# Kernel optimization log

Hardware: AMD Instinct MI355X
Metric: run time of the kernel (lower is better)

## Reference

```python
import jax, jax.numpy as jnp
import numpy as np

B, C, H, W, N = 4, 128, 240, 320, 1024
LEVEL = 8.0          # scaling[0] = 4 * img_scale with img_scale=2
E1_LAMDA = 1.0
E2_LAMDA = 2.0 / 7.0
GN_LAMDA = 0.3
EPS = 1e-9


def extract_features(f, coords):
    # f: (B,C,H,W); coords: (B,N,2) float pixel coords as (x, y)
    Bf, Cf, Hf, Wf = f.shape
    x = coords[..., 0]
    y = coords[..., 1]
    x0 = jnp.floor(x)
    y0 = jnp.floor(y)
    wx = (x - x0)[:, None, :]          # (B,1,N)
    wy = (y - y0)[:, None, :]
    x0i = jnp.clip(x0.astype(jnp.int32), 0, Wf - 1)
    x1i = jnp.clip(x0i + 1, 0, Wf - 1)
    y0i = jnp.clip(y0.astype(jnp.int32), 0, Hf - 1)
    y1i = jnp.clip(y0i + 1, 0, Hf - 1)

    def g(fm, yi, xi):                 # fm: (C,H,W), yi/xi: (N,)
        return fm[:, yi, xi]           # (C,N)

    v00 = jax.vmap(g)(f, y0i, x0i)
    v01 = jax.vmap(g)(f, y0i, x1i)
    v10 = jax.vmap(g)(f, y1i, x0i)
    v11 = jax.vmap(g)(f, y1i, x1i)
    out = (v00 * (1 - wx) * (1 - wy) + v01 * wx * (1 - wy)
           + v10 * (1 - wx) * wy + v11 * wx * wy)          # (B,C,N)
    return out.transpose(0, 2, 1).reshape(Bf * coords.shape[1], Cf)


def l2_normalize(f):
    n = jnp.linalg.norm(f, axis=1, keepdims=True)
    return f / jnp.maximum(n, 1e-12)


def torch_gradient(f):
    # central differences with edge replication; gx = d/dx (width), gy = d/dy (height)
    fpx = jnp.pad(f, ((0, 0), (0, 0), (0, 0), (1, 1)), mode='edge')
    fpy = jnp.pad(f, ((0, 0), (0, 0), (1, 1), (0, 0)), mode='edge')
    gx = 0.5 * (fpx[..., 2:] - fpx[..., :-2])
    gy = 0.5 * (fpy[..., 2:, :] - fpy[..., :-2, :])
    return gx, gy


def compute_gn_loss(f_t, fb, ub, noise):
    Bn, Nn, _ = ub.shape
    xs = (2.0 * noise - 1.0) + ub                   # uniform(-1,1) jitter
    f_s = extract_features(fb, xs)
    f_t = l2_normalize(f_t)
    f_s = l2_normalize(f_s)
    r = f_s - f_t                                   # (BN, C)
    gx, gy = torch_gradient(fb)
    Jx = extract_features(gx, xs)                   # (BN, C)
    Jy = extract_features(gy, xs)
    J = jnp.stack([Jx, Jy], axis=-1)                # (BN, C, 2)
    Hm = jnp.einsum('bci,bcj->bij', J, J) + EPS * jnp.eye(2, dtype=J.dtype)
    b = jnp.einsum('bci,bc->bi', J, r)[..., None]   # (BN, 2, 1)
    # closed-form 2x2 inverse
    a = Hm[:, 0, 0]; bb = Hm[:, 0, 1]; c = Hm[:, 1, 0]; d = Hm[:, 1, 1]
    det = a * d - bb * c
    Hinv = jnp.stack([jnp.stack([d, -bb], -1),
                      jnp.stack([-c, a], -1)], -2) / det[:, None, None]
    miu = xs.reshape(Bn * Nn, 2, 1) - Hinv @ b
    diff = (ub.reshape(Bn * Nn, 2, 1) - miu)[..., 0]          # (BN, 2)
    e1 = 0.5 * jnp.sum(jnp.einsum('bi,bij,bj->b', diff, Hm, diff))
    log_det = jnp.log(det)
    e2 = Bn * Nn * jnp.log(jnp.asarray(2.0 * np.pi, dtype=det.dtype)) - 0.5 * jnp.sum(log_det)
    e = E1_LAMDA * e1 + E2_LAMDA * e2
    return e, e1, e2


def setup_inputs() -> dict:
    key = jax.random.key(0)
    k = jax.random.split(key, 7)
    F_a = jax.random.normal(k[0], (B, C, H, W), dtype=jnp.float32)
    F_b = jax.random.normal(k[1], (B, C, H, W), dtype=jnp.float32)
    # full-resolution match coords, safely inside the map after /LEVEL
    xa = jax.random.uniform(k[2], (B, N)) * (W - 5) * LEVEL + 2 * LEVEL
    ya = jax.random.uniform(k[3], (B, N)) * (H - 5) * LEVEL + 2 * LEVEL
    xb = jax.random.uniform(k[4], (B, N)) * (W - 5) * LEVEL + 2 * LEVEL
    yb = jax.random.uniform(k[5], (B, N)) * (H - 5) * LEVEL + 2 * LEVEL
    matches_a = jnp.stack([xa, ya], axis=-1)
    matches_b = jnp.stack([xb, yb], axis=-1)
    noise = jax.random.uniform(k[6], (B, N, 2), dtype=jnp.float32)
    return {"F_a": F_a, "F_b": F_b, "matches_a": matches_a,
            "matches_b": matches_b, "noise": noise}


def reference(F_a, F_b, matches_a, matches_b, noise):
    f_t = extract_features(F_a, matches_a / LEVEL)
    e, e1, e2 = compute_gn_loss(f_t, F_b, matches_b / LEVEL, noise)
    return GN_LAMDA * e, e1, e2
```

## Files before the change

kernel.cpp:

```cpp
#include <hip/hip_runtime.h>
#include <math.h>

#define B_  4
#define C_  128
#define H_  240
#define W_  320
#define N_  1024
#define NPTS (B_ * N_)
#define HW_ (H_ * W_)

typedef float f4 __attribute__((ext_vector_type(4)));
typedef float f2 __attribute__((ext_vector_type(2)));

__device__ __forceinline__ f4 load4(const float* p) {
    f4 v;
    __builtin_memcpy(&v, p, 16);
    return v;
}
__device__ __forceinline__ f2 load2(const float* p) {
    f2 v;
    __builtin_memcpy(&v, p, 8);
    return v;
}

__device__ __forceinline__ float wave_reduce(float v) {
    #pragma unroll
    for (int off = 32; off > 0; off >>= 1)
        v += __shfl_xor(v, off, 64);
    return v;
}

__global__ __launch_bounds__(256) void gn_point_kernel(
    const float* __restrict__ Fa, const float* __restrict__ Fb,
    const float* __restrict__ ma, const float* __restrict__ mb,
    const float* __restrict__ noise,
    float* __restrict__ ws_e1, float* __restrict__ ws_ld)
{
    const int wid  = threadIdx.x >> 6;
    const int lane = threadIdx.x & 63;
    const int p = (blockIdx.x << 2) | wid;
    const int b = p >> 10;

    const float inv_level = 0.125f;
    const float xa  = ma[p * 2 + 0] * inv_level;
    const float ya  = ma[p * 2 + 1] * inv_level;
    const float ubx = mb[p * 2 + 0] * inv_level;
    const float uby = mb[p * 2 + 1] * inv_level;
    const float xs  = 2.0f * noise[p * 2 + 0] - 1.0f + ubx;
    const float ys  = 2.0f * noise[p * 2 + 1] - 1.0f + uby;

    const float ax0f = floorf(xa), ay0f = floorf(ya);
    const float awx = xa - ax0f, awy = ya - ay0f;
    const int ax0 = min(max((int)ax0f, 0), W_ - 2);
    const int ay0 = min(max((int)ay0f, 0), H_ - 2);

    const float bx0f = floorf(xs), by0f = floorf(ys);
    const float wx = xs - bx0f, wy = ys - by0f;
    const int x0 = min(max((int)bx0f, 1), W_ - 3);
    const int y0 = min(max((int)by0f, 1), H_ - 3);
    const int xm = x0 - 1;
    const int ym = y0 - 1;
    const int y1 = y0 + 1;
    const int yp = y0 + 2;

    const int o_y0 = y0 * W_ + xm;
    const int o_y1 = y1 * W_ + xm;
    const int o_ym = ym * W_ + x0;
    const int o_yp = yp * W_ + x0;
    const int o_a0 = ay0 * W_ + ax0;
    const int o_a1 = (ay0 + 1) * W_ + ax0;

    const size_t plane = ((size_t)b * C_ + lane) * HW_;
    const float* __restrict__ fa0 = Fa + plane;
    const float* __restrict__ fa1 = fa0 + (size_t)64 * HW_;
    const float* __restrict__ fb0 = Fb + plane;
    const float* __restrict__ fb1 = fb0 + (size_t)64 * HW_;

    const f4 row0_0 = load4(fb0 + o_y0);
    const f4 row1_0 = load4(fb0 + o_y1);
    const f2 rm_0   = load2(fb0 + o_ym);
    const f2 rp_0   = load2(fb0 + o_yp);
    const f2 a0_0   = load2(fa0 + o_a0);
    const f2 a1_0   = load2(fa0 + o_a1);

    const f4 row0_1 = load4(fb1 + o_y0);
    const f4 row1_1 = load4(fb1 + o_y1);
    const f2 rm_1   = load2(fb1 + o_ym);
    const f2 rp_1   = load2(fb1 + o_yp);
    const f2 a0_1   = load2(fa1 + o_a0);
    const f2 a1_1   = load2(fa1 + o_a1);

    const float aw00 = (1.f - awx) * (1.f - awy);
    const float aw01 = awx * (1.f - awy);
    const float aw10 = (1.f - awx) * awy;
    const float aw11 = awx * awy;
    const float w00 = (1.f - wx) * (1.f - wy);
    const float w01 = wx * (1.f - wy);
    const float w10 = (1.f - wx) * wy;
    const float w11 = wx * wy;

    float vals[9];
    #pragma unroll
    for (int k = 0; k < 9; ++k) vals[k] = 0.f;

    #pragma unroll
    for (int ch = 0; ch < 2; ++ch) {
        const f4 row0 = ch ? row0_1 : row0_0;
        const f4 row1 = ch ? row1_1 : row1_0;
        const f2 rm   = ch ? rm_1   : rm_0;
        const f2 rp   = ch ? rp_1   : rp_0;
        const f2 a0   = ch ? a0_1   : a0_0;
        const f2 a1   = ch ? a1_1   : a1_0;

        const float ft = a0.x * aw00 + a0.y * aw01 + a1.x * aw10 + a1.y * aw11;
        const float fs = row0.y * w00 + row0.z * w01 + row1.y * w10 + row1.z * w11;
        const float jx = 0.5f * ((row0.z - row0.x) * w00 + (row0.w - row0.y) * w01
                               + (row1.z - row1.x) * w10 + (row1.w - row1.y) * w11);
        const float jy = 0.5f * ((row1.y - rm.x) * w00 + (row1.z - rm.y) * w01
                               + (rp.x - row0.y) * w10 + (rp.y - row0.z) * w11);

        vals[0] += ft * ft;
        vals[1] += fs * fs;
        vals[2] += jx * fs;
        vals[3] += jx * ft;
        vals[4] += jy * fs;
        vals[5] += jy * ft;
        vals[6] += jx * jx;
        vals[7] += jx * jy;
        vals[8] += jy * jy;
    }

    #pragma unroll
    for (int k = 0; k < 9; ++k)
        vals[k] = wave_reduce(vals[k]);

    if (lane == 0) {
        const float nt = fmaxf(sqrtf(vals[0]), 1e-12f);
        const float ns = fmaxf(sqrtf(vals[1]), 1e-12f);
        const float b0 = vals[2] / ns - vals[3] / nt;
        const float b1 = vals[4] / ns - vals[5] / nt;
        const float H00 = vals[6] + 1e-9f;
        const float H01 = vals[7];
        const float H11 = vals[8] + 1e-9f;
        const float det = H00 * H11 - H01 * H01;
        const float inv = 1.0f / det;
        const float u0 = (H11 * b0 - H01 * b1) * inv;
        const float u1 = (H00 * b1 - H01 * b0) * inv;
        const float d0 = (ubx - xs) + u0;
        const float d1 = (uby - ys) + u1;
        const float quad = d0 * (H00 * d0 + H01 * d1) + d1 * (H01 * d0 + H11 * d1);
        ws_e1[p] = 0.5f * quad;
        ws_ld[p] = logf(det);
    }
}

__global__ __launch_bounds__(256) void gn_reduce_kernel(
    const float* __restrict__ ws_e1, const float* __restrict__ ws_ld,
    float* __restrict__ out)
{
    __shared__ double sm1[256];
    __shared__ double sm2[256];
    double a1 = 0.0, a2 = 0.0;
    for (int i = threadIdx.x; i < NPTS; i += 256) {
        a1 += (double)ws_e1[i];
        a2 += (double)ws_ld[i];
    }
    sm1[threadIdx.x] = a1;
    sm2[threadIdx.x] = a2;
    __syncthreads();
    for (int s = 128; s > 0; s >>= 1) {
        if (threadIdx.x < s) {
            sm1[threadIdx.x] += sm1[threadIdx.x + s];
            sm2[threadIdx.x] += sm2[threadIdx.x + s];
        }
        __syncthreads();
    }
    if (threadIdx.x == 0) {
        const double e1 = sm1[0];
        const double sum_ld = sm2[0];
        const double log2pi = (double)logf(6.283185307179586f);
        const double e2 = (double)NPTS * log2pi - 0.5 * sum_ld;
        const double e = 1.0 * e1 + (2.0 / 7.0) * e2;
        out[0] = (float)(0.3 * e);
        out[1] = (float)e1;
        out[2] = (float)e2;
    }
}

extern "C" void kernel_launch(void* const* d_in, const int* in_sizes, int n_in,
                              void* d_out, int out_size, void* d_ws, size_t ws_size,
                              hipStream_t stream) {
    const float* Fa    = (const float*)d_in[0];
    const float* Fb    = (const float*)d_in[1];
    const float* ma    = (const float*)d_in[2];
    const float* mb    = (const float*)d_in[3];
    const float* noise = (const float*)d_in[4];
    float* out = (float*)d_out;

    float* ws_e1 = (float*)d_ws;
    float* ws_ld = ws_e1 + NPTS;

    gn_point_kernel<<<NPTS / 4, 256, 0, stream>>>(Fa, Fb, ma, mb, noise, ws_e1, ws_ld);
    gn_reduce_kernel<<<1, 256, 0, stream>>>(ws_e1, ws_ld, out);
}
```

Before: 70.33 us.

## Sort points by batch and row for locality; split channels across two waves

A new single-block kernel counting-sorts the 4096 points by (batch, sampled row) and writes a permutation. The point kernel then processes points in that order, so neighbouring blocks gather from nearby rows of the feature maps and may get better cache reuse. Each point now uses two waves of 64 channels each, halving per-thread loads and doubling the block count, and the two partial results are combined through shared memory. The cost is an extra kernel launch with a serial single-block sort, plus a block barrier in the point kernel.

```diff
diff --git a/kernel.cpp b/kernel.cpp
--- a/kernel.cpp
+++ b/kernel.cpp
@@ -8,19 +8,16 @@
 #define N_  1024
 #define NPTS (B_ * N_)
 #define HW_ (H_ * W_)
+#define NBINS 960
 
 typedef float f4 __attribute__((ext_vector_type(4)));
 typedef float f2 __attribute__((ext_vector_type(2)));
 
 __device__ __forceinline__ f4 load4(const float* p) {
-    f4 v;
-    __builtin_memcpy(&v, p, 16);
-    return v;
+    f4 v; __builtin_memcpy(&v, p, 16); return v;
 }
 __device__ __forceinline__ f2 load2(const float* p) {
-    f2 v;
-    __builtin_memcpy(&v, p, 8);
-    return v;
+    f2 v; __builtin_memcpy(&v, p, 8); return v;
 }
 
 __device__ __forceinline__ float wave_reduce(float v) {
@@ -30,16 +27,66 @@
     return v;
 }
 
+__global__ __launch_bounds__(1024) void gn_sort_kernel(
+    const float* __restrict__ mb, const float* __restrict__ noise,
+    int* __restrict__ perm)
+{
+    __shared__ int hist[NBINS];
+    __shared__ int cursor[NBINS];
+    for (int i = threadIdx.x; i < NBINS; i += 1024) hist[i] = 0;
+    __syncthreads();
+
+    int mykey[4];
+    #pragma unroll
+    for (int k = 0; k < 4; ++k) {
+        const int p = threadIdx.x + (k << 10);
+        const float uby = mb[p * 2 + 1] * 0.125f;
+        const float ys  = 2.0f * noise[p * 2 + 1] - 1.0f + uby;
+        const int y0 = min(max((int)floorf(ys), 1), H_ - 3);
+        mykey[k] = (p >> 10) * H_ + y0;
+        atomicAdd(&hist[mykey[k]], 1);
+    }
+    __syncthreads();
+
+    if (threadIdx.x < 64) {
+        const int lane = threadIdx.x;
+        const int base = lane * 15;
+        int loc[15];
+        int s = 0;
+        #pragma unroll
+        for (int i = 0; i < 15; ++i) { loc[i] = s; s += hist[base + i]; }
+        int incl = s;
+        #pragma unroll
+        for (int off = 1; off < 64; off <<= 1) {
+            const int v = __shfl_up(incl, off, 64);
+            if (lane >= off) incl += v;
+        }
+        const int excl = incl - s;
+        #pragma unroll
+        for (int i = 0; i < 15; ++i) cursor[base + i] = excl + loc[i];
+    }
+    __syncthreads();
+
+    #pragma unroll
+    for (int k = 0; k < 4; ++k) {
+        const int p = threadIdx.x + (k << 10);
+        const int pos = atomicAdd(&cursor[mykey[k]], 1);
+        perm[pos] = p;
+    }
+}
+
 __global__ __launch_bounds__(256) void gn_point_kernel(
     const float* __restrict__ Fa, const float* __restrict__ Fb,
     const float* __restrict__ ma, const float* __restrict__ mb,
-    const float* __restrict__ noise,
+    const float* __restrict__ noise, const int* __restrict__ perm,
     float* __restrict__ ws_e1, float* __restrict__ ws_ld)
 {
     const int wid  = threadIdx.x >> 6;
     const int lane = threadIdx.x & 63;
-    const int p = (blockIdx.x << 2) | wid;
+    const int slot = (blockIdx.x << 1) | (wid >> 1);
+    const int p = perm[slot];
     const int b = p >> 10;
+    const int c = ((wid & 1) << 6) | lane;
 
     const float inv_level = 0.125f;
     const float xa  = ma[p * 2 + 0] * inv_level;
@@ -59,36 +106,24 @@
     const int x0 = min(max((int)bx0f, 1), W_ - 3);
     const int y0 = min(max((int)by0f, 1), H_ - 3);
     const int xm = x0 - 1;
-    const int ym = y0 - 1;
-    const int y1 = y0 + 1;
-    const int yp = y0 + 2;
 
     const int o_y0 = y0 * W_ + xm;
-    const int o_y1 = y1 * W_ + xm;
-    const int o_ym = ym * W_ + x0;
-    const int o_yp = yp * W_ + x0;
+    const int o_y1 = (y0 + 1) * W_ + xm;
+    const int o_ym = (y0 - 1) * W_ + x0;
+    const int o_yp = (y0 + 2) * W_ + x0;
     const int o_a0 = ay0 * W_ + ax0;
     const int o_a1 = (ay0 + 1) * W_ + ax0;
 
-    const size_t plane = ((size_t)b * C_ + lane) * HW_;
-    const float* __restrict__ fa0 = Fa + plane;
-    const float* __restrict__ fa1 = fa0 + (size_t)64 * HW_;
-    const float* __restrict__ fb0 = Fb + plane;
-    const float* __restrict__ fb1 = fb0 + (size_t)64 * HW_;
-
-    const f4 row0_0 = load4(fb0 + o_y0);
-    const f4 row1_0 = load4(fb0 + o_y1);
-    const f2 rm_0   = load2(fb0 + o_ym);
-    const f2 rp_0   = load2(fb0 + o_yp);
-    const f2 a0_0   = load2(fa0 + o_a0);
-    const f2 a1_0   = load2(fa0 + o_a1);
-
-    const f4 row0_1 = load4(fb1 + o_y0);
-    const f4 row1_1 = load4(fb1 + o_y1);
-    const f2 rm_1   = load2(fb1 + o_ym);
-    const f2 rp_1   = load2(fb1 + o_yp);
-    const f2 a0_1   = load2(fa1 + o_a0);
-    const f2 a1_1   = load2(fa1 + o_a1);
+    const size_t plane = ((size_t)b * C_ + c) * HW_;
+    const float* __restrict__ fa = Fa + plane;
+    const float* __restrict__ fb = Fb + plane;
+
+    const f4 row0 = load4(fb + o_y0);
+    const f4 row1 = load4(fb + o_y1);
+    const f2 rm   = load2(fb + o_ym);
+    const f2 rp   = load2(fb + o_yp);
+    const f2 a0   = load2(fa + o_a0);
+    const f2 a1   = load2(fa + o_a1);
 
     const float aw00 = (1.f - awx) * (1.f - awy);
     const float aw01 = awx * (1.f - awy);
@@ -99,49 +134,47 @@
     const float w10 = (1.f - wx) * wy;
     const float w11 = wx * wy;
 
+    const float ft = a0.x * aw00 + a0.y * aw01 + a1.x * aw10 + a1.y * aw11;
+    const float fs = row0.y * w00 + row0.z * w01 + row1.y * w10 + row1.z * w11;
+    const float jx = 0.5f * ((row0.z - row0.x) * w00 + (row0.w - row0.y) * w01
+                           + (row1.z - row1.x) * w10 + (row1.w - row1.y) * w11);
+    const float jy = 0.5f * ((row1.y - rm.x) * w00 + (row1.z - rm.y) * w01
+                           + (rp.x - row0.y) * w10 + (rp.y - row0.z) * w11);
+
     float vals[9];
-    #pragma unroll
-    for (int k = 0; k < 9; ++k) vals[k] = 0.f;
-
-    #pragma unroll
-    for (int ch = 0; ch < 2; ++ch) {
-        const f4 row0 = ch ? row0_1 : row0_0;
-        const f4 row1 = ch ? row1_1 : row1_0;
-        const f2 rm   = ch ? rm_1   : rm_0;
-        const f2 rp   = ch ? rp_1   : rp_0;
-        const f2 a0   = ch ? a0_1   : a0_0;
-        const f2 a1   = ch ? a1_1   : a1_0;
-
-        const float ft = a0.x * aw00 + a0.y * aw01 + a1.x * aw10 + a1.y * aw11;
-        const float fs = row0.y * w00 + row0.z * w01 + row1.y * w10 + row1.z * w11;
-        const float jx = 0.5f * ((row0.z - row0.x) * w00 + (row0.w - row0.y) * w01
-                               + (row1.z - row1.x) * w10 + (row1.w - row1.y) * w11);
-        const float jy = 0.5f * ((row1.y - rm.x) * w00 + (row1.z - rm.y) * w01
-                               + (rp.x - row0.y) * w10 + (rp.y - row0.z) * w11);
-
-        vals[0] += ft * ft;
-        vals[1] += fs * fs;
-        vals[2] += jx * fs;
-        vals[3] += jx * ft;
-        vals[4] += jy * fs;
-        vals[5] += jy * ft;
-        vals[6] += jx * jx;
-        vals[7] += jx * jy;
-        vals[8] += jy * jy;
-    }
+    vals[0] = ft * ft;
+    vals[1] = fs * fs;
+    vals[2] = jx * fs;
+    vals[3] = jx * ft;
+    vals[4] = jy * fs;
+    vals[5] = jy * ft;
+    vals[6] = jx * jx;
+    vals[7] = jx * jy;
+    vals[8] = jy * jy;
 
     #pragma unroll
     for (int k = 0; k < 9; ++k)
         vals[k] = wave_reduce(vals[k]);
 
+    __shared__ float sm[4][9];
     if (lane == 0) {
-        const float nt = fmaxf(sqrtf(vals[0]), 1e-12f);
-        const float ns = fmaxf(sqrtf(vals[1]), 1e-12f);
-        const float b0 = vals[2] / ns - vals[3] / nt;
-        const float b1 = vals[4] / ns - vals[5] / nt;
-        const float H00 = vals[6] + 1e-9f;
-        const float H01 = vals[7];
-        const float H11 = vals[8] + 1e-9f;
+        #pragma unroll
+        for (int k = 0; k < 9; ++k) sm[wid][k] = vals[k];
+    }
+    __syncthreads();
+
+    if ((threadIdx.x & 127) == 0) {
+        float s[9];
+        #pragma unroll
+        for (int k = 0; k < 9; ++k) s[k] = sm[wid][k] + sm[wid + 1][k];
+
+        const float nt = fmaxf(sqrtf(s[0]), 1e-12f);
+        const float ns = fmaxf(sqrtf(s[1]), 1e-12f);
+        const float b0 = s[2] / ns - s[3] / nt;
+        const float b1 = s[4] / ns - s[5] / nt;
+        const float H00 = s[6] + 1e-9f;
+        const float H01 = s[7];
+        const float H11 = s[8] + 1e-9f;
         const float det = H00 * H11 - H01 * H01;
         const float inv = 1.0f / det;
         const float u0 = (H11 * b0 - H01 * b1) * inv;
@@ -199,7 +232,10 @@
 
     float* ws_e1 = (float*)d_ws;
     float* ws_ld = ws_e1 + NPTS;
-
-    gn_point_kernel<<<NPTS / 4, 256, 0, stream>>>(Fa, Fb, ma, mb, noise, ws_e1, ws_ld);
+    int*   perm  = (int*)(ws_ld + NPTS);
+
+    gn_sort_kernel<<<1, 1024, 0, stream>>>(mb, noise, perm);
+    gn_point_kernel<<<NPTS / 2, 256, 0, stream>>>(Fa, Fb, ma, mb, noise, perm,
+                                                  ws_e1, ws_ld);
     gn_reduce_kernel<<<1, 256, 0, stream>>>(ws_e1, ws_ld, out);
 }
```

Result: slower. 76.93 us (+9.4%).
